# Kernel tuning notes

Hardware: AMD Instinct MI355X
Metric: run time of the kernel (lower is better)

The kernel has to match this reference:

```python
import jax, jax.numpy as jnp
import numpy as np

D_MODEL = 1024
NUM_HEADS = 16
D_K = D_MODEL // NUM_HEADS
LN_EPS = 1e-5


def setup_inputs() -> dict:
    key = jax.random.key(0)
    ks = jax.random.split(key, 16)
    B, SQ, SK = 2, 2048, 2048
    s = 1.0 / np.sqrt(D_MODEL)
    inp = {
        "query": jax.random.normal(ks[0], (B, SQ, D_MODEL), jnp.float32),
        "key": jax.random.normal(ks[1], (B, SK, D_MODEL), jnp.float32),
        "value": jax.random.normal(ks[2], (B, SK, D_MODEL), jnp.float32),
        "mask": jax.random.randint(ks[3], (B, SQ, SK), 0, 2, jnp.int32),
        "w_q": jax.random.normal(ks[4], (D_MODEL, D_MODEL), jnp.float32) * s,
        "b_q": jnp.zeros((D_MODEL,), jnp.float32),
        "w_k": jax.random.normal(ks[5], (D_MODEL, D_MODEL), jnp.float32) * s,
        "b_k": jnp.zeros((D_MODEL,), jnp.float32),
        "w_v": jax.random.normal(ks[6], (D_MODEL, D_MODEL), jnp.float32) * s,
        "b_v": jnp.zeros((D_MODEL,), jnp.float32),
        "w_o": jax.random.normal(ks[7], (D_MODEL, D_MODEL), jnp.float32) * s,
        "b_o": jnp.zeros((D_MODEL,), jnp.float32),
        "ln_gamma": jnp.ones((D_MODEL,), jnp.float32),
        "ln_beta": jnp.zeros((D_MODEL,), jnp.float32),
    }
    return inp


def _split_heads(x):
    B, S, _ = x.shape
    return x.reshape(B, S, NUM_HEADS, D_K).transpose(0, 2, 1, 3)  # [B,H,S,Dk]


def reference(query, key, value, mask, w_q, b_q, w_k, b_k, w_v, b_v, w_o, b_o, ln_gamma, ln_beta):
    residual = query
    # torch Linear: y = x @ W.T + b
    Q = _split_heads(jnp.einsum('bsd,ed->bse', query, w_q) + b_q)
    K = _split_heads(jnp.einsum('bsd,ed->bse', key, w_k) + b_k)
    V = _split_heads(jnp.einsum('bsd,ed->bse', value, w_v) + b_v)
    scores = jnp.einsum('bhqd,bhkd->bhqk', Q, K) / jnp.sqrt(jnp.float32(D_K))
    scores = jnp.where(mask[:, None, :, :] == 0, jnp.float32(-1e9), scores)
    attn = jax.nn.softmax(scores, axis=-1)
    # dropout: eval mode (identity)
    ctx = jnp.einsum('bhqk,bhkd->bhqd', attn, V)
    B, H, SQ, Dk = ctx.shape
    ctx = ctx.transpose(0, 2, 1, 3).reshape(B, SQ, D_MODEL)
    out = jnp.einsum('bsd,ed->bse', ctx, w_o) + b_o + residual
    mu = jnp.mean(out, axis=-1, keepdims=True)
    var = jnp.mean(jnp.square(out - mu), axis=-1, keepdims=True)
    out = (out - mu) * jax.lax.rsqrt(var + LN_EPS) * ln_gamma + ln_beta
    return out
```

## Files before the change

kernel.cpp:

```cpp
#include <hip/hip_runtime.h>

typedef unsigned short u16;
typedef __attribute__((ext_vector_type(8))) short bf16x8;
typedef __attribute__((ext_vector_type(4))) float f32x4;

#define LOG2E 1.4426950408889634f
#define QSCALE (LOG2E / 8.0f)

__device__ __forceinline__ u16 f2bf(float f) {
  union { float f; unsigned u; } v; v.f = f;
  unsigned r = v.u + 0x7fffu + ((v.u >> 16) & 1u);
  return (u16)(r >> 16);
}

__device__ __forceinline__ void gload_lds16(const void* g, void* l) {
  __builtin_amdgcn_global_load_lds(
      (const __attribute__((address_space(1))) unsigned int*)(unsigned long long)g,
      (__attribute__((address_space(3))) unsigned int*)(unsigned int)(unsigned long long)l,
      16, 0, 0);
}

__global__ __launch_bounds__(256) void prep_kernel(
    const float* __restrict__ q, const float* __restrict__ k, const float* __restrict__ v,
    const float* __restrict__ wq, const float* __restrict__ wk, const float* __restrict__ wv,
    const float* __restrict__ wo, const int* __restrict__ mask,
    u16* __restrict__ Xq, u16* __restrict__ Xk, u16* __restrict__ Xv,
    u16* __restrict__ Wq, u16* __restrict__ Wk, u16* __restrict__ Wv, u16* __restrict__ Wo,
    unsigned long long* __restrict__ Mp) {
  const int bx = blockIdx.x;
  if (bx < 16384) {
    const float* src; u16* dst; float sc; int idx;
    if (bx < 12288) {
      int seg = bx >> 12;
      idx = (bx & 4095) * 256 + threadIdx.x;
      src = seg == 0 ? q : (seg == 1 ? k : v);
      dst = seg == 0 ? Xq : (seg == 1 ? Xk : Xv);
      sc = 1.f;
    } else {
      int t = bx - 12288, seg = t >> 10;
      idx = (t & 1023) * 256 + threadIdx.x;
      src = seg == 0 ? wq : (seg == 1 ? wk : (seg == 2 ? wv : wo));
      dst = seg == 0 ? Wq : (seg == 1 ? Wk : (seg == 2 ? Wv : Wo));
      sc = seg == 0 ? QSCALE : 1.f;
    }
    float4 x = ((const float4*)src)[idx];
    ushort4 o;
    o.x = f2bf(x.x * sc); o.y = f2bf(x.y * sc);
    o.z = f2bf(x.z * sc); o.w = f2bf(x.w * sc);
    ((ushort4*)dst)[idx] = o;
  } else {
    int gw = (((bx - 16384) * 256) + threadIdx.x) >> 6;
    int lane = threadIdx.x & 63;
    for (int w = gw; w < 131072; w += 16384) {
      int m = mask[(size_t)w * 64 + lane];
      unsigned long long b = __ballot(m != 0);
      if (lane == 0) Mp[w] = b;
    }
  }
}

__global__ __launch_bounds__(256, 3) void gemm_kernel(
    const u16* __restrict__ Xq, const u16* __restrict__ Xk, const u16* __restrict__ Xv,
    const u16* __restrict__ Wq, const u16* __restrict__ Wk, const u16* __restrict__ Wv,
    const u16* __restrict__ Wo, const u16* __restrict__ Ctx,
    const float* __restrict__ bq, const float* __restrict__ bk, const float* __restrict__ bv,
    u16* __restrict__ Qd, u16* __restrict__ Kd, u16* __restrict__ Vtd, float* __restrict__ outp,
    int mode_base) {
  __shared__ __align__(16) u16 SH[17408];
  u16* As = SH;
  u16* Bs = SH + 4096;
  const int mode = mode_base + blockIdx.z;
  const int tid = threadIdx.x;
  const int wid = tid >> 6, l = tid & 63, quad = l >> 4, ln = l & 15;
  const int wm = wid >> 1, wn = wid & 1;

  const u16 *A, *B; const float* bias;
  if (mode == 0)      { A = Wq; B = Xq;  bias = bq; }
  else if (mode == 1) { A = Wk; B = Xk;  bias = bk; }
  else if (mode == 2) { A = Xv; B = Wv;  bias = bv; }
  else                { A = Wo; B = Ctx; bias = bq; }
  int mBase, nBase;
  if (mode == 2) { mBase = blockIdx.x * 128; nBase = blockIdx.y * 128; }
  else           { mBase = blockIdx.y * 128; nBase = blockIdx.x * 128; }

  const u16* Ag = A + (size_t)mBase * 1024;
  const u16* Bg = B + (size_t)nBase * 1024;

  f32x4 acc[4][4] = {};

  for (int k0 = 0; k0 < 1024; k0 += 32) {
    if (k0) __syncthreads();
    {
      int i0 = tid, i1 = tid + 256;
      gload_lds16(Ag + (size_t)(i0 & 127) * 1024 + k0 + (i0 >> 7) * 8, &As[i0 * 8]);
      gload_lds16(Ag + (size_t)(i1 & 127) * 1024 + k0 + (i1 >> 7) * 8, &As[i1 * 8]);
      gload_lds16(Bg + (size_t)(i0 & 127) * 1024 + k0 + (i0 >> 7) * 8, &Bs[i0 * 8]);
      gload_lds16(Bg + (size_t)(i1 & 127) * 1024 + k0 + (i1 >> 7) * 8, &Bs[i1 * 8]);
    }
    __syncthreads();
    bf16x8 af[4], bf[4];
#pragma unroll
    for (int i = 0; i < 4; ++i)
      af[i] = *(const bf16x8*)&As[(quad * 128 + wm * 64 + i * 16 + ln) * 8];
#pragma unroll
    for (int j = 0; j < 4; ++j)
      bf[j] = *(const bf16x8*)&Bs[(quad * 128 + wn * 64 + j * 16 + ln) * 8];
#pragma unroll
    for (int i = 0; i < 4; ++i)
#pragma unroll
      for (int j = 0; j < 4; ++j)
        acc[i][j] = __builtin_amdgcn_mfma_f32_16x16x32_bf16(af[i], bf[j], acc[i][j], 0, 0, 0);
  }

  __syncthreads();

  if (mode <= 1) {
    const float bscale = (mode == 0) ? QSCALE : 1.0f;
#pragma unroll
    for (int i = 0; i < 4; ++i) {
      int f0 = wm * 64 + i * 16 + quad * 4;
      float4 bb = *(const float4*)(bias + mBase + f0);
#pragma unroll
      for (int j = 0; j < 4; ++j) {
        int sl = wn * 64 + j * 16 + ln;
        f32x4 v = acc[i][j];
        ushort4 o;
        o.x = f2bf(v[0] + bb.x * bscale); o.y = f2bf(v[1] + bb.y * bscale);
        o.z = f2bf(v[2] + bb.z * bscale); o.w = f2bf(v[3] + bb.w * bscale);
        *(ushort4*)&SH[sl * 136 + f0] = o;
      }
    }
    __syncthreads();
    u16* dstQK = (mode == 0) ? Qd : Kd;
#pragma unroll
    for (int p = 0; p < 8; ++p) {
      int sl = p * 16 + (tid >> 4);
      int fl = (tid & 15) * 8;
      uint4 w = *(const uint4*)&SH[sl * 136 + fl];
      int s = nBase + sl, f = mBase + fl;
      int h = f >> 6, d = f & 63, b = s >> 11, sr = s & 2047;
      *(uint4*)(dstQK + (((size_t)(b * 16 + h) * 2048 + sr) * 64 + d)) = w;
    }
  } else if (mode == 2) {
#pragma unroll
    for (int j = 0; j < 4; ++j) {
      int fl = wn * 64 + j * 16 + ln;
      float bb = bias[nBase + fl];
#pragma unroll
      for (int i = 0; i < 4; ++i) {
        int s0 = wm * 64 + i * 16 + quad * 4;
        f32x4 v = acc[i][j];
        ushort4 o;
        o.x = f2bf(v[0] + bb); o.y = f2bf(v[1] + bb);
        o.z = f2bf(v[2] + bb); o.w = f2bf(v[3] + bb);
        *(ushort4*)&SH[fl * 136 + s0] = o;
      }
    }
    __syncthreads();
#pragma unroll
    for (int p = 0; p < 8; ++p) {
      int fl = p * 16 + (tid >> 4);
      int sl = (tid & 15) * 8;
      uint4 w = *(const uint4*)&SH[fl * 136 + sl];
      int f = nBase + fl, s = mBase + sl;
      int h = f >> 6, d = f & 63, b = s >> 11, sr = s & 2047;
      *(uint4*)(Vtd + (((size_t)(b * 16 + h) * 64 + d) * 2048 + sr)) = w;
    }
  } else {
    float* ES = (float*)SH;
#pragma unroll
    for (int h2 = 0; h2 < 2; ++h2) {
      if (h2) __syncthreads();
      if (wn == h2) {
#pragma unroll
        for (int i = 0; i < 4; ++i) {
          int f0 = wm * 64 + i * 16 + quad * 4;
#pragma unroll
          for (int j = 0; j < 4; ++j) {
            int sl = j * 16 + ln;
            f32x4 v = acc[i][j];
            float4 o; o.x = v[0]; o.y = v[1]; o.z = v[2]; o.w = v[3];
            *(float4*)&ES[sl * 132 + f0] = o;
          }
        }
      }
      __syncthreads();
#pragma unroll
      for (int p = 0; p < 8; ++p) {
        int sl = p * 8 + (tid >> 5);
        int fl = (tid & 31) * 4;
        float4 w = *(const float4*)&ES[sl * 132 + fl];
        int s = nBase + h2 * 64 + sl;
        *(float4*)(outp + (size_t)s * 1024 + mBase + fl) = w;
      }
    }
  }
}

__global__ __launch_bounds__(256, 2) void attn_kernel(
    const u16* __restrict__ Qg, const u16* __restrict__ Kg, const u16* __restrict__ Vtg,
    const unsigned* __restrict__ Mp, u16* __restrict__ ctx) {
  __shared__ __align__(16) u16 Ks0[8192];
  __shared__ __align__(16) u16 Ks1[8192];
  __shared__ __align__(16) u16 Vs0[8192];
  __shared__ __align__(16) u16 Vs1[8192];
  __shared__ __align__(16) u16 Ps[8192];
  const int tid = threadIdx.x;
  const int wid = tid >> 6, l = tid & 63, quad = l >> 4, ln = l & 15;
  const int q4 = quad * 4;
  const int L = blockIdx.x;
  const int bh = (L & 7) + 8 * (L >> 7);
  const int b = bh >> 4, h = bh & 15;
  const int qBase = ((L >> 3) & 15) * 128;
  const int wq = wid * 32;
  const int sw = (ln & 7) << 3;

  bf16x8 qf[2][2];
#pragma unroll
  for (int qt = 0; qt < 2; ++qt)
#pragma unroll
    for (int kc = 0; kc < 2; ++kc)
      qf[qt][kc] = *(const bf16x8*)(Qg + (((size_t)bh * 2048 + qBase + wq + qt * 16 + ln) * 64 +
                                          kc * 32 + quad * 8));

  f32x4 oacc[2][4] = {};
  f32x4 lsum[2] = {};
  const bf16x8 vone = {(short)0x3F80, (short)0x3F80, (short)0x3F80, (short)0x3F80,
                       (short)0x3F80, (short)0x3F80, (short)0x3F80, (short)0x3F80};

  const unsigned* mrow[2];
  mrow[0] = Mp + ((size_t)b * 2048 + qBase + wq + ln) * 64;
  mrow[1] = mrow[0] + 16 * 64;

  const u16* KgB = Kg + (size_t)bh * 2048 * 64;
  const u16* VgB = Vtg + (size_t)bh * 64 * 2048;

#define STAGE_TILE(KS, VS, t_)                                                  \
  do {                                                                          \
    const int kvB_ = (t_) * 128;                                                \
    _Pragma("unroll")                                                           \
    for (int r_ = 0; r_ < 4; ++r_) {                                            \
      int c_ = r_ * 256 + tid;                                                  \
      gload_lds16(KgB + (size_t)(kvB_ + (c_ & 127)) * 64 + (c_ >> 7) * 8,       \
                  &KS[c_ * 8]);                                                 \
      gload_lds16(VgB + (size_t)(c_ & 63) * 2048 + kvB_ + (c_ >> 6) * 8,        \
                  &VS[c_ * 8]);                                                 \
    }                                                                           \
  } while (0)

#define COMPUTE_TILE(KS, VS, it_)                                                         \
  do {                                                                                    \
    unsigned ww[2][4];                                                                    \
    {                                                                                     \
      uint4 m0 = *(const uint4*)(mrow[0] + (it_) * 4);                                    \
      uint4 m1 = *(const uint4*)(mrow[1] + (it_) * 4);                                    \
      ww[0][0] = m0.x; ww[0][1] = m0.y; ww[0][2] = m0.z; ww[0][3] = m0.w;                 \
      ww[1][0] = m1.x; ww[1][1] = m1.y; ww[1][2] = m1.z; ww[1][3] = m1.w;                 \
    }                                                                                     \
    _Pragma("unroll")                                                                     \
    for (int hf = 0; hf < 2; ++hf) {                                                      \
      f32x4 s[4][2];                                                                      \
      __builtin_amdgcn_s_setprio(1);                                                      \
      _Pragma("unroll")                                                                   \
      for (int m2 = 0; m2 < 4; ++m2) {                                                    \
        int mt = hf * 4 + m2;                                                             \
        bf16x8 k0 = *(const bf16x8*)&KS[((0 + quad) * 128 + mt * 16 + ln) * 8];           \
        bf16x8 k1 = *(const bf16x8*)&KS[((4 + quad) * 128 + mt * 16 + ln) * 8];           \
        _Pragma("unroll")                                                                 \
        for (int qt = 0; qt < 2; ++qt) {                                                  \
          f32x4 z = {0.f, 0.f, 0.f, 0.f};                                                 \
          z = __builtin_amdgcn_mfma_f32_16x16x32_bf16(k0, qf[qt][0], z, 0, 0, 0);         \
          s[m2][qt] = __builtin_amdgcn_mfma_f32_16x16x32_bf16(k1, qf[qt][1], z, 0, 0, 0); \
        }                                                                                 \
      }                                                                                   \
      __builtin_amdgcn_s_setprio(0);                                                      \
      uint2 pk[4][2];                                                                     \
      _Pragma("unroll")                                                                   \
      for (int qt = 0; qt < 2; ++qt)                                                      \
        _Pragma("unroll")                                                                 \
        for (int m2 = 0; m2 < 4; ++m2) {                                                  \
          int mt = hf * 4 + m2;                                                           \
          unsigned nib = (ww[qt][mt >> 1] >> ((mt & 1) * 16 + q4)) & 0xFu;                \
          float p0 = __builtin_amdgcn_exp2f((nib & 1u) ? s[m2][qt][0] : -1e30f);          \
          float p1 = __builtin_amdgcn_exp2f((nib & 2u) ? s[m2][qt][1] : -1e30f);          \
          float p2 = __builtin_amdgcn_exp2f((nib & 4u) ? s[m2][qt][2] : -1e30f);          \
          float p3 = __builtin_amdgcn_exp2f((nib & 8u) ? s[m2][qt][3] : -1e30f);          \
          pk[m2][qt].x = __builtin_amdgcn_perm(__float_as_uint(p1),                       \
                                               __float_as_uint(p0), 0x07060302u);         \
          pk[m2][qt].y = __builtin_amdgcn_perm(__float_as_uint(p3),                       \
                                               __float_as_uint(p2), 0x07060302u);         \
        }                                                                                 \
              \
      _Pragma("unroll")                                                                   \
      for (int qt = 0; qt < 2; ++qt) {                                                    \
        int qrow = wq + qt * 16 + ln;                                                     \
        _Pragma("unroll")                                                                 \
        for (int m2 = 0; m2 < 4; ++m2)                                                    \
          *(uint2*)&Ps[(qrow * 64 + m2 * 16 + q4) ^ sw] = pk[m2][qt];                     \
      }                                                                                   \
      __builtin_amdgcn_s_setprio(1);                                                      \
      _Pragma("unroll")                                                                   \
      for (int k2 = 0; k2 < 2; ++k2) {                                                    \
        int kc2 = hf * 2 + k2;                                                            \
        bf16x8 aP[2];                                                                     \
        _Pragma("unroll")                                                                 \
        for (int qt = 0; qt < 2; ++qt)                                                    \
          aP[qt] = *(const bf16x8*)&Ps[((wq + qt * 16 + ln) * 64 + k2 * 32 + quad * 8) ^ sw]; \
        _Pragma("unroll")                                                                 \
        for (int nt = 0; nt < 4; ++nt) {                                                  \
          bf16x8 bV = *(const bf16x8*)&VS[((kc2 * 4 + quad) * 64 + nt * 16 + ln) * 8];    \
          _Pragma("unroll")                                                               \
          for (int qt = 0; qt < 2; ++qt)                                                  \
            oacc[qt][nt] = __builtin_amdgcn_mfma_f32_16x16x32_bf16(aP[qt], bV, oacc[qt][nt], 0, 0, 0); \
        }                                                                                 \
        _Pragma("unroll")                                                                 \
        for (int qt = 0; qt < 2; ++qt)                                                    \
          lsum[qt] = __builtin_amdgcn_mfma_f32_16x16x32_bf16(aP[qt], vone, lsum[qt], 0, 0, 0); \
      }                                                                                   \
      __builtin_amdgcn_s_setprio(0);                                                      \
    }                                                                                     \
  } while (0)

  STAGE_TILE(Ks0, Vs0, 0);
#pragma unroll 1
  for (int it2 = 0; it2 < 8; ++it2) {
    __syncthreads();
    STAGE_TILE(Ks1, Vs1, 2 * it2 + 1);
    COMPUTE_TILE(Ks0, Vs0, 2 * it2);
    __syncthreads();
    if (it2 < 7) STAGE_TILE(Ks0, Vs0, 2 * it2 + 2);
    COMPUTE_TILE(Ks1, Vs1, 2 * it2 + 1);
  }
#undef STAGE_TILE
#undef COMPUTE_TILE

  __syncthreads();
#pragma unroll
  for (int qt = 0; qt < 2; ++qt)
#pragma unroll
    for (int r = 0; r < 4; ++r) {
      float il = 1.0f / lsum[qt][r];
      int q = wq + qt * 16 + q4 + r;
#pragma unroll
      for (int nt = 0; nt < 4; ++nt)
        Ps[q * 64 + nt * 16 + ln] = f2bf(oacc[qt][nt][r] * il);
    }
  __syncthreads();
#pragma unroll
  for (int r = 0; r < 4; ++r) {
    int c = r * 256 + tid;
    int q = c >> 3, ch = c & 7;
    *(uint4*)(ctx + ((size_t)(b * 2048 + qBase + q) * 1024 + h * 64 + ch * 8)) =
        *(const uint4*)&Ps[q * 64 + ch * 8];
  }
}

__global__ __launch_bounds__(256) void ln_kernel(const float* __restrict__ x,
                                                 const float* __restrict__ resid,
                                                 const float* __restrict__ bo,
                                                 const float* __restrict__ gamma,
                                                 const float* __restrict__ beta,
                                                 float* __restrict__ out) {
  __shared__ float red[8];
  const int tid = threadIdx.x;
  const size_t row = blockIdx.x;
  float4 v = ((const float4*)(x + row * 1024))[tid];
  const float4 rr = ((const float4*)(resid + row * 1024))[tid];
  const float4 bb = ((const float4*)bo)[tid];
  v.x += rr.x + bb.x; v.y += rr.y + bb.y; v.z += rr.z + bb.z; v.w += rr.w + bb.w;
  float s1 = v.x + v.y + v.z + v.w;
  float s2 = v.x * v.x + v.y * v.y + v.z * v.z + v.w * v.w;
#pragma unroll
  for (int o = 32; o >= 1; o >>= 1) {
    s1 += __shfl_xor(s1, o);
    s2 += __shfl_xor(s2, o);
  }
  if ((tid & 63) == 0) { red[(tid >> 6) * 2] = s1; red[(tid >> 6) * 2 + 1] = s2; }
  __syncthreads();
  s1 = red[0] + red[2] + red[4] + red[6];
  s2 = red[1] + red[3] + red[5] + red[7];
  float mu = s1 * (1.f / 1024.f);
  float var = s2 * (1.f / 1024.f) - mu * mu;
  float inv = rsqrtf(var + 1e-5f);
  float4 g = ((const float4*)gamma)[tid];
  float4 be = ((const float4*)beta)[tid];
  float4 o;
  o.x = (v.x - mu) * inv * g.x + be.x;
  o.y = (v.y - mu) * inv * g.y + be.y;
  o.z = (v.z - mu) * inv * g.z + be.z;
  o.w = (v.w - mu) * inv * g.w + be.w;
  ((float4*)(out + row * 1024))[tid] = o;
}

extern "C" void kernel_launch(void* const* d_in, const int* in_sizes, int n_in,
                              void* d_out, int out_size, void* d_ws, size_t ws_size,
                              hipStream_t stream) {
  const float* query = (const float*)d_in[0];
  const float* key   = (const float*)d_in[1];
  const float* value = (const float*)d_in[2];
  const int*   mask  = (const int*)d_in[3];
  const float* w_q = (const float*)d_in[4];
  const float* b_q = (const float*)d_in[5];
  const float* w_k = (const float*)d_in[6];
  const float* b_k = (const float*)d_in[7];
  const float* w_v = (const float*)d_in[8];
  const float* b_v = (const float*)d_in[9];
  const float* w_o = (const float*)d_in[10];
  const float* b_o = (const float*)d_in[11];
  const float* ln_g = (const float*)d_in[12];
  const float* ln_b = (const float*)d_in[13];
  float* out = (float*)d_out;

  char* ws = (char*)d_ws;
  u16* Xq = (u16*)(ws + ((size_t)0 << 20));
  u16* Xk = (u16*)(ws + ((size_t)8 << 20));
  u16* Xv = (u16*)(ws + ((size_t)16 << 20));
  float* outpre = (float*)(ws + ((size_t)8 << 20));
  u16* Wq = (u16*)(ws + ((size_t)24 << 20));
  u16* Wk = (u16*)(ws + ((size_t)26 << 20));
  u16* Wv = (u16*)(ws + ((size_t)28 << 20));
  u16* Wo = (u16*)(ws + ((size_t)30 << 20));
  u16* Qd = (u16*)(ws + ((size_t)32 << 20));
  u16* Kd = (u16*)(ws + ((size_t)40 << 20));
  u16* Vtd = (u16*)(ws + ((size_t)48 << 20));
  unsigned long long* Mp = (unsigned long long*)(ws + ((size_t)56 << 20));
  u16* ctx = Xq;

  prep_kernel<<<20480, 256, 0, stream>>>(query, key, value, w_q, w_k, w_v, w_o, mask,
                                         Xq, Xk, Xv, Wq, Wk, Wv, Wo, Mp);
  gemm_kernel<<<dim3(32, 8, 3), 256, 0, stream>>>(Xq, Xk, Xv, Wq, Wk, Wv, Wo, ctx,
      b_q, b_k, b_v, Qd, Kd, Vtd, outpre, 0);
  attn_kernel<<<dim3(512), 256, 0, stream>>>(Qd, Kd, Vtd, (const unsigned*)Mp, ctx);
  gemm_kernel<<<dim3(32, 8, 1), 256, 0, stream>>>(Xq, Xk, Xv, Wq, Wk, Wv, Wo, ctx,
      b_q, b_k, b_v, Qd, Kd, Vtd, outpre, 3);
  ln_kernel<<<4096, 256, 0, stream>>>(outpre, query, b_o, ln_g, ln_b, out);
}
```

Measured before the change: 312.2 us.

## Split attention block across eight waves with sixteen query rows each

The attention kernel now runs 512 threads (eight waves) per block instead of 256, and each wave handles 16 query rows rather than 32. Per-wave register state (Q fragments, accumulators, softmax sums) is halved, staging loads are spread over more threads, and launch bounds request higher occupancy. The aim is more latency hiding and better MFMA issue. The cost is that each K/V fragment read from LDS now feeds half as many MFMAs, which doubles LDS read traffic per unit of work, and block-wide barriers now involve more waves.

```diff
diff --git a/kernel.cpp b/kernel.cpp
--- a/kernel.cpp
+++ b/kernel.cpp
@@ -197,7 +197,7 @@
   }
 }
 
-__global__ __launch_bounds__(256, 2) void attn_kernel(
+__global__ __launch_bounds__(512, 4) void attn_kernel(
     const u16* __restrict__ Qg, const u16* __restrict__ Kg, const u16* __restrict__ Vtg,
     const unsigned* __restrict__ Mp, u16* __restrict__ ctx) {
   __shared__ __align__(16) u16 Ks0[8192];
@@ -212,25 +212,21 @@
   const int bh = (L & 7) + 8 * (L >> 7);
   const int b = bh >> 4, h = bh & 15;
   const int qBase = ((L >> 3) & 15) * 128;
-  const int wq = wid * 32;
+  const int wq = wid * 16;
   const int sw = (ln & 7) << 3;
 
-  bf16x8 qf[2][2];
-#pragma unroll
-  for (int qt = 0; qt < 2; ++qt)
-#pragma unroll
-    for (int kc = 0; kc < 2; ++kc)
-      qf[qt][kc] = *(const bf16x8*)(Qg + (((size_t)bh * 2048 + qBase + wq + qt * 16 + ln) * 64 +
-                                          kc * 32 + quad * 8));
-
-  f32x4 oacc[2][4] = {};
-  f32x4 lsum[2] = {};
+  bf16x8 qf[2];
+#pragma unroll
+  for (int kc = 0; kc < 2; ++kc)
+    qf[kc] = *(const bf16x8*)(Qg + (((size_t)bh * 2048 + qBase + wq + ln) * 64 +
+                                    kc * 32 + quad * 8));
+
+  f32x4 oacc[4] = {};
+  f32x4 lsum = {};
   const bf16x8 vone = {(short)0x3F80, (short)0x3F80, (short)0x3F80, (short)0x3F80,
                        (short)0x3F80, (short)0x3F80, (short)0x3F80, (short)0x3F80};
 
-  const unsigned* mrow[2];
-  mrow[0] = Mp + ((size_t)b * 2048 + qBase + wq + ln) * 64;
-  mrow[1] = mrow[0] + 16 * 64;
+  const unsigned* mrow = Mp + ((size_t)b * 2048 + qBase + wq + ln) * 64;
 
   const u16* KgB = Kg + (size_t)bh * 2048 * 64;
   const u16* VgB = Vtg + (size_t)bh * 64 * 2048;
@@ -239,8 +235,8 @@
   do {                                                                          \
     const int kvB_ = (t_) * 128;                                                \
     _Pragma("unroll")                                                           \
-    for (int r_ = 0; r_ < 4; ++r_) {                                            \
-      int c_ = r_ * 256 + tid;                                                  \
+    for (int r_ = 0; r_ < 2; ++r_) {                                            \
+      int c_ = r_ * 512 + tid;                                                  \
       gload_lds16(KgB + (size_t)(kvB_ + (c_ & 127)) * 64 + (c_ >> 7) * 8,       \
                   &KS[c_ * 8]);                                                 \
       gload_lds16(VgB + (size_t)(c_ & 63) * 2048 + kvB_ + (c_ >> 6) * 8,        \
@@ -250,72 +246,54 @@
 
 #define COMPUTE_TILE(KS, VS, it_)                                                         \
   do {                                                                                    \
-    unsigned ww[2][4];                                                                    \
+    unsigned ww[4];                                                                       \
     {                                                                                     \
-      uint4 m0 = *(const uint4*)(mrow[0] + (it_) * 4);                                    \
-      uint4 m1 = *(const uint4*)(mrow[1] + (it_) * 4);                                    \
-      ww[0][0] = m0.x; ww[0][1] = m0.y; ww[0][2] = m0.z; ww[0][3] = m0.w;                 \
-      ww[1][0] = m1.x; ww[1][1] = m1.y; ww[1][2] = m1.z; ww[1][3] = m1.w;                 \
+      uint4 m0 = *(const uint4*)(mrow + (it_) * 4);                                       \
+      ww[0] = m0.x; ww[1] = m0.y; ww[2] = m0.z; ww[3] = m0.w;                             \
     }                                                                                     \
     _Pragma("unroll")                                                                     \
     for (int hf = 0; hf < 2; ++hf) {                                                      \
-      f32x4 s[4][2];                                                                      \
+      f32x4 s[4];                                                                         \
       __builtin_amdgcn_s_setprio(1);                                                      \
       _Pragma("unroll")                                                                   \
       for (int m2 = 0; m2 < 4; ++m2) {                                                    \
         int mt = hf * 4 + m2;                                                             \
         bf16x8 k0 = *(const bf16x8*)&KS[((0 + quad) * 128 + mt * 16 + ln) * 8];           \
         bf16x8 k1 = *(const bf16x8*)&KS[((4 + quad) * 128 + mt * 16 + ln) * 8];           \
-        _Pragma("unroll")                                                                 \
-        for (int qt = 0; qt < 2; ++qt) {                                                  \
-          f32x4 z = {0.f, 0.f, 0.f, 0.f};                                                 \
-          z = __builtin_amdgcn_mfma_f32_16x16x32_bf16(k0, qf[qt][0], z, 0, 0, 0);         \
-          s[m2][qt] = __builtin_amdgcn_mfma_f32_16x16x32_bf16(k1, qf[qt][1], z, 0, 0, 0); \
-        }                                                                                 \
+        f32x4 z = {0.f, 0.f, 0.f, 0.f};                                                   \
+        z = __builtin_amdgcn_mfma_f32_16x16x32_bf16(k0, qf[0], z, 0, 0, 0);               \
+        s[m2] = __builtin_amdgcn_mfma_f32_16x16x32_bf16(k1, qf[1], z, 0, 0, 0);           \
       }                                                                                   \
       __builtin_amdgcn_s_setprio(0);                                                      \
-      uint2 pk[4][2];                                                                     \
+      uint2 pk[4];                                                                        \
       _Pragma("unroll")                                                                   \
-      for (int qt = 0; qt < 2; ++qt)                                                      \
-        _Pragma("unroll")                                                                 \
-        for (int m2 = 0; m2 < 4; ++m2) {                                                  \
-          int mt = hf * 4 + m2;                                                           \
-          unsigned nib = (ww[qt][mt >> 1] >> ((mt & 1) * 16 + q4)) & 0xFu;                \
-          float p0 = __builtin_amdgcn_exp2f((nib & 1u) ? s[m2][qt][0] : -1e30f);          \
-          float p1 = __builtin_amdgcn_exp2f((nib & 2u) ? s[m2][qt][1] : -1e30f);          \
-          float p2 = __builtin_amdgcn_exp2f((nib & 4u) ? s[m2][qt][2] : -1e30f);          \
-          float p3 = __builtin_amdgcn_exp2f((nib & 8u) ? s[m2][qt][3] : -1e30f);          \
-          pk[m2][qt].x = __builtin_amdgcn_perm(__float_as_uint(p1),                       \
-                                               __float_as_uint(p0), 0x07060302u);         \
-          pk[m2][qt].y = __builtin_amdgcn_perm(__float_as_uint(p3),                       \
-                                               __float_as_uint(p2), 0x07060302u);         \
-        }                                                                                 \
+      for (int m2 = 0; m2 < 4; ++m2) {                                                    \
+        int mt = hf * 4 + m2;                                                             \
+        unsigned nib = (ww[mt >> 1] >> ((mt & 1) * 16 + q4)) & 0xFu;                      \
+        float p0 = __builtin_amdgcn_exp2f((nib & 1u) ? s[m2][0] : -1e30f);                \
+        float p1 = __builtin_amdgcn_exp2f((nib & 2u) ? s[m2][1] : -1e30f);                \
+        float p2 = __builtin_amdgcn_exp2f((nib & 4u) ? s[m2][2] : -1e30f);                \
+        float p3 = __builtin_amdgcn_exp2f((nib & 8u) ? s[m2][3] : -1e30f);                \
+        pk[m2].x = __builtin_amdgcn_perm(__float_as_uint(p1), __float_as_uint(p0),        \
+                                         0x07060302u);                                    \
+        pk[m2].y = __builtin_amdgcn_perm(__float_as_uint(p3), __float_as_uint(p2),        \
+                                         0x07060302u);                                    \
+      }                                                                                   \
               \
       _Pragma("unroll")                                                                   \
-      for (int qt = 0; qt < 2; ++qt) {                                                    \
-        int qrow = wq + qt * 16 + ln;                                                     \
-        _Pragma("unroll")                                                                 \
-        for (int m2 = 0; m2 < 4; ++m2)                                                    \
-          *(uint2*)&Ps[(qrow * 64 + m2 * 16 + q4) ^ sw] = pk[m2][qt];                     \
-      }                                                                                   \
+      for (int m2 = 0; m2 < 4; ++m2)                                                      \
+        *(uint2*)&Ps[(((wq + ln) * 64) + m2 * 16 + q4) ^ sw] = pk[m2];                    \
       __builtin_amdgcn_s_setprio(1);                                                      \
       _Pragma("unroll")                                                                   \
       for (int k2 = 0; k2 < 2; ++k2) {                                                    \
         int kc2 = hf * 2 + k2;                                                            \
-        bf16x8 aP[2];                                                                     \
-        _Pragma("unroll")                                                                 \
-        for (int qt = 0; qt < 2; ++qt)                                                    \
-          aP[qt] = *(const bf16x8*)&Ps[((wq + qt * 16 + ln) * 64 + k2 * 32 + quad * 8) ^ sw]; \
+        bf16x8 aP = *(const bf16x8*)&Ps[(((wq + ln) * 64) + k2 * 32 + quad * 8) ^ sw];    \
         _Pragma("unroll")                                                                 \
         for (int nt = 0; nt < 4; ++nt) {                                                  \
           bf16x8 bV = *(const bf16x8*)&VS[((kc2 * 4 + quad) * 64 + nt * 16 + ln) * 8];    \
-          _Pragma("unroll")                                                               \
-          for (int qt = 0; qt < 2; ++qt)                                                  \
-            oacc[qt][nt] = __builtin_amdgcn_mfma_f32_16x16x32_bf16(aP[qt], bV, oacc[qt][nt], 0, 0, 0); \
+          oacc[nt] = __builtin_amdgcn_mfma_f32_16x16x32_bf16(aP, bV, oacc[nt], 0, 0, 0);  \
         }                                                                                 \
-        _Pragma("unroll")                                                                 \
-        for (int qt = 0; qt < 2; ++qt)                                                    \
-          lsum[qt] = __builtin_amdgcn_mfma_f32_16x16x32_bf16(aP[qt], vone, lsum[qt], 0, 0, 0); \
+        lsum = __builtin_amdgcn_mfma_f32_16x16x32_bf16(aP, vone, lsum, 0, 0, 0);          \
       }                                                                                   \
       __builtin_amdgcn_s_setprio(0);                                                      \
     }                                                                                     \
@@ -336,19 +314,17 @@
 
   __syncthreads();
 #pragma unroll
-  for (int qt = 0; qt < 2; ++qt)
-#pragma unroll
-    for (int r = 0; r < 4; ++r) {
-      float il = 1.0f / lsum[qt][r];
-      int q = wq + qt * 16 + q4 + r;
-#pragma unroll
-      for (int nt = 0; nt < 4; ++nt)
-        Ps[q * 64 + nt * 16 + ln] = f2bf(oacc[qt][nt][r] * il);
-    }
+  for (int r = 0; r < 4; ++r) {
+    float il = 1.0f / lsum[r];
+    int q = wq + q4 + r;
+#pragma unroll
+    for (int nt = 0; nt < 4; ++nt)
+      Ps[q * 64 + nt * 16 + ln] = f2bf(oacc[nt][r] * il);
+  }
   __syncthreads();
 #pragma unroll
-  for (int r = 0; r < 4; ++r) {
-    int c = r * 256 + tid;
+  for (int r = 0; r < 2; ++r) {
+    int c = r * 512 + tid;
     int q = c >> 3, ch = c & 7;
     *(uint4*)(ctx + ((size_t)(b * 2048 + qBase + q) * 1024 + h * 64 + ch * 8)) =
         *(const uint4*)&Ps[q * 64 + ch * 8];
@@ -430,7 +406,7 @@
                                          Xq, Xk, Xv, Wq, Wk, Wv, Wo, Mp);
   gemm_kernel<<<dim3(32, 8, 3), 256, 0, stream>>>(Xq, Xk, Xv, Wq, Wk, Wv, Wo, ctx,
       b_q, b_k, b_v, Qd, Kd, Vtd, outpre, 0);
-  attn_kernel<<<dim3(512), 256, 0, stream>>>(Qd, Kd, Vtd, (const unsigned*)Mp, ctx);
+  attn_kernel<<<dim3(512), 512, 0, stream>>>(Qd, Kd, Vtd, (const unsigned*)Mp, ctx);
   gemm_kernel<<<dim3(32, 8, 1), 256, 0, stream>>>(Xq, Xk, Xv, Wq, Wk, Wv, Wo, ctx,
       b_q, b_k, b_v, Qd, Kd, Vtd, outpre, 3);
   ln_kernel<<<4096, 256, 0, stream>>>(outpre, query, b_o, ln_g, ln_b, out);
```

After: 308.6 us. No clear change (-1.1%).
